# Kernel optimization log

Hardware: AMD Instinct MI355X
Metric: run time of the kernel (lower is better)

## Reference

```python
import jax, jax.numpy as jnp
import numpy as np

D = 128  # input_depth == output_depth
NUM_NODES_PATTERN = np.tile(np.array([32, 48, 64, 96], dtype=np.int64), 64)  # G=256 graphs


def _build_indices(nn_np):
    """Per pair-entry (row-major within each n_g x n_g block): global row node,
    global col node, graph id, diagonal mask; plus per-node graph id / size."""
    G = len(nn_np)
    offs = np.zeros(G, dtype=np.int64)
    offs[1:] = np.cumsum(nn_np)[:-1]
    rows_l, cols_l, g_l, diag_l = [], [], [], []
    for gi, (n, o) in enumerate(zip(nn_np, offs)):
        i = np.repeat(np.arange(n, dtype=np.int64), n)  # row index within block
        j = np.tile(np.arange(n, dtype=np.int64), n)    # col index within block
        rows_l.append(o + i)
        cols_l.append(o + j)
        g_l.append(np.full(n * n, gi, dtype=np.int64))
        diag_l.append(i == j)
    rows = np.concatenate(rows_l)
    cols = np.concatenate(cols_l)
    g_edge = np.concatenate(g_l)
    diag = np.concatenate(diag_l)
    g_node = np.repeat(np.arange(G, dtype=np.int64), nn_np)  # graph of each node
    n_node = np.repeat(nn_np, nn_np)                          # n_g of each node
    N = int(nn_np.sum())
    return rows, cols, g_edge, diag, g_node, n_node, N, G


def setup_inputs() -> dict:
    key = jax.random.key(0)
    nn_np = NUM_NODES_PATTERN
    E = int(np.sum(nn_np ** 2))  # 1,064,960 pair entries
    N = int(nn_np.sum())         # 15,360 nodes
    k1, k2, k3 = jax.random.split(key, 3)
    x = jax.random.normal(k1, (E, D), dtype=jnp.float32)
    coeffs = jax.random.normal(k2, (D, D, 5), dtype=jnp.float32) * float(np.sqrt(2.0) / (D + D))
    bias = jnp.zeros((1, D), dtype=jnp.float32)
    edges_index = jax.random.randint(k3, (2, E), 0, N, dtype=jnp.int64)  # unused by the layer
    num_nodes = jnp.asarray(nn_np)
    return {"x": x, "coeffs": coeffs, "bias": bias,
            "edges_index": edges_index, "num_nodes": num_nodes}


def reference(x, coeffs, bias, edges_index, num_nodes):
    # edges_index is unused, matching the original forward.
    nn_np = np.asarray(num_nodes)
    rows, cols, g_edge, diag, g_node, n_node, N, G = _build_indices(nn_np)
    seg = jax.ops.segment_sum
    diag_m = jnp.asarray(diag)[:, None].astype(x.dtype)  # [E,1]
    n = jnp.asarray(n_node).astype(x.dtype)[:, None]     # [N,1] block size per node

    op1 = seg(x * diag_m, jnp.asarray(rows), num_segments=N)          # diag part (unnormalized)
    op3 = seg(x, jnp.asarray(rows), num_segments=N) / n               # row sums / n
    op4 = seg(x, jnp.asarray(cols), num_segments=N) / n               # col sums / n
    diag_g = seg(x * diag_m, jnp.asarray(g_edge), num_segments=G)     # [G,d] trace per graph
    all_g = seg(x, jnp.asarray(g_edge), num_segments=G)               # [G,d] total sum per graph
    gn = jnp.asarray(g_node)
    op2 = diag_g[gn] / n                                              # trace broadcast / n
    op5 = all_g[gn] / (n * n)                                         # total broadcast / n^2

    ops = jnp.stack([op1, op2, op3, op4, op5], axis=2)                # [N, d, 5]
    out = jnp.einsum('dsb,ndb->ns', coeffs, ops) + bias               # [N, output_depth]
    return out
```

## Files before the change

### kernel.cpp

```cpp
#include <hip/hip_runtime.h>

#define D 128


__device__ __forceinline__ void f4add(float4& a, const float4& b) {
    a.x += b.x; a.y += b.y; a.z += b.z; a.w += b.w;
}

__device__ __forceinline__ void f4shflxor_add(float4& a, int mask) {
    a.x += __shfl_xor(a.x, mask);
    a.y += __shfl_xor(a.y, mask);
    a.z += __shfl_xor(a.z, mask);
    a.w += __shfl_xor(a.w, mask);
}

template<int N>
__device__ __forceinline__ void run_class(const float* __restrict__ x,
                                          long ebase, int o, int gidx, int chunk,
                                          float* __restrict__ diagG,
                                          float* __restrict__ rowG,
                                          float* __restrict__ colG,
                                          float* __restrict__ trG,
                                          float* __restrict__ totG,
                                          float4* rowpart ) {
    const int tid = threadIdx.x;
    const int L   = tid & 63;
    const int w   = tid >> 6;
    const int j0  = tid >> 3;
    const int f4  = tid & 7;
    const float invn = 1.0f / (float)N;
    constexpr bool TWO = (N > 64);
    const bool act0 = (j0 < N);
    const bool act1 = TWO && (j0 + 64 < N);

    const float4* x4 = reinterpret_cast<const float4*>(x);
    const long e0 = (ebase + j0) * 32 + chunk * 8 + f4;
    const long e1 = e0 + 64L * 32;
    const long istride = (long)N * 32;

    float4 c0 = {0,0,0,0}, c1 = {0,0,0,0};

    for (int t0 = 0; t0 < N; t0 += 16) {
#pragma unroll 8
        for (int r = 0; r < 16; ++r) {
            const int i = t0 + r;
            float4 v0 = {0,0,0,0}, v1 = {0,0,0,0};
            if (act0) v0 = x4[e0 + (long)i * istride];
            if (TWO && act1) v1 = x4[e1 + (long)i * istride];
            f4add(c0, v0);
            if (TWO) f4add(c1, v1);
            float4 s = v0;
            if (TWO) f4add(s, v1);
            f4shflxor_add(s, 8);
            f4shflxor_add(s, 16);
            f4shflxor_add(s, 32);
            if (L < 8) rowpart[(r * 8 + w) * 8 + L] = s;
        }
        __syncthreads();
        {
            const int r  = tid >> 5;
            const int dd = tid & 31;
            const float* rp = reinterpret_cast<const float*>(rowpart);
            float acc = 0.f;
#pragma unroll
            for (int w2 = 0; w2 < 8; ++w2) acc += rp[r * 256 + w2 * 32 + dd];
            rowG[(long)(o + t0 + r) * D + chunk * 32 + dd] = acc * invn;
        }
        __syncthreads();
    }

    float4 d0 = {0,0,0,0}, d1 = {0,0,0,0};
    if (act0) d0 = x4[e0 + (long)j0 * istride];
    if (TWO && act1) d1 = x4[e1 + (long)(j0 + 64) * istride];

    float4* diag4 = reinterpret_cast<float4*>(diagG);
    float4* col4  = reinterpret_cast<float4*>(colG);
    if (act0) {
        diag4[(long)(o + j0) * 32 + chunk * 8 + f4] = d0;
        col4 [(long)(o + j0) * 32 + chunk * 8 + f4] = c0;
    }
    if (TWO && act1) {
        diag4[(long)(o + j0 + 64) * 32 + chunk * 8 + f4] = d1;
        col4 [(long)(o + j0 + 64) * 32 + chunk * 8 + f4] = c1;
    }

    float4 td = d0; if (TWO) f4add(td, d1);
    float4 tc = c0; if (TWO) f4add(tc, c1);
    f4shflxor_add(td, 8);  f4shflxor_add(tc, 8);
    f4shflxor_add(td, 16); f4shflxor_add(tc, 16);
    f4shflxor_add(td, 32); f4shflxor_add(tc, 32);
    if (L < 8) {
        rowpart[w * 8 + L]      = td;
        rowpart[64 + w * 8 + L] = tc;
    }
    __syncthreads();
    float4* tr4  = reinterpret_cast<float4*>(trG);
    float4* tot4 = reinterpret_cast<float4*>(totG);
    if (tid < 8) {
        float4 a = {0,0,0,0};
#pragma unroll
        for (int w2 = 0; w2 < 8; ++w2) f4add(a, rowpart[w2 * 8 + tid]);
        tr4[gidx * 32 + chunk * 8 + tid] = a;
    } else if (tid < 16) {
        const int f = tid - 8;
        float4 a = {0,0,0,0};
#pragma unroll
        for (int w2 = 0; w2 < 8; ++w2) f4add(a, rowpart[64 + w2 * 8 + f]);
        tot4[gidx * 32 + chunk * 8 + f] = a;
    }
}

__global__ __launch_bounds__(512) void k1_reduce(const float* __restrict__ x,
                                                 float* __restrict__ diagG,
                                                 float* __restrict__ rowG,
                                                 float* __restrict__ colG,
                                                 float* __restrict__ trG,
                                                 float* __restrict__ totG) {
    __shared__ float4 rowpart[1024];

    const int b  = blockIdx.x;
    const int bb = b & 255;
    const int k  = bb >> 2;
    const int chunk = bb & 3;

    if (b < 256) {
        run_class<96>(x, 16640L * k + 7424, 240 * k + 144, 4 * k + 3, chunk, diagG, rowG, colG, trG, totG, rowpart);
    } else if (b < 512) {
        run_class<64>(x, 16640L * k + 3328, 240 * k + 80, 4 * k + 2, chunk, diagG, rowG, colG, trG, totG, rowpart);
    } else if (b < 768) {
        run_class<48>(x, 16640L * k + 1024, 240 * k + 32, 4 * k + 1, chunk, diagG, rowG, colG, trG, totG, rowpart);
    } else {
        run_class<32>(x, 16640L * k, 240 * k, 4 * k, chunk, diagG, rowG, colG, trG, totG, rowpart);
    }
}

__global__ void k0_transpose(const float* __restrict__ coeffs, float* __restrict__ Wt) {
    int d = blockIdx.x;
    int s = threadIdx.x;
    const float* cp = coeffs + ((long)d * D + s) * 5;
#pragma unroll
    for (int b = 0; b < 5; ++b) Wt[b * (D * D) + d * D + s] = cp[b];
}

__global__ __launch_bounds__(128) void k2_pg(const float* __restrict__ trG,
                                             const float* __restrict__ totG,
                                             const float* __restrict__ Wt,
                                             const float* __restrict__ bias,
                                             float* __restrict__ pg) {
    __shared__ float tr[D], tt[D];
    const int ns_[4] = {32, 48, 64, 96};
    int g = blockIdx.x;
    int c = g & 3;
    float invn = 1.0f / (float)ns_[c];

    int s = threadIdx.x;
    tr[s] = trG[g * D + s] * invn;
    tt[s] = totG[g * D + s] * invn * invn;
    __syncthreads();

    const float* W1 = Wt + 1 * D * D;
    const float* W4 = Wt + 4 * D * D;
    float acc = 0.f;
#pragma unroll 4
    for (int dd = 0; dd < D; ++dd)
        acc += W1[dd * D + s] * tr[dd] + W4[dd * D + s] * tt[dd];
    pg[g * D + s] = bias[s] + acc;
}

__global__ __launch_bounds__(512) void k3_gemm(const float* __restrict__ diagG,
                                               const float* __restrict__ rowG,
                                               const float* __restrict__ colG,
                                               const float* __restrict__ Wt,
                                               const float* __restrict__ pg,
                                               float* __restrict__ out) {
    __shared__ float ash[3][64][D];
    __shared__ int gish[64];
    const int nd0 = blockIdx.x * 64;
    const int tid = threadIdx.x;

    for (int idx = tid; idx < 64 * D; idx += 512) {
        int nn = idx >> 7;
        int d  = idx & 127;
        int nd = nd0 + nn;
        int p  = nd / 240;
        int r  = nd - p * 240;
        int c, n;
        if (r < 32)       { c = 0; n = 32; }
        else if (r < 80)  { c = 1; n = 48; }
        else if (r < 144) { c = 2; n = 64; }
        else              { c = 3; n = 96; }
        float invn = 1.0f / (float)n;
        ash[0][nn][d] = diagG[(long)nd * D + d];
        ash[1][nn][d] = rowG[(long)nd * D + d];
        ash[2][nn][d] = colG[(long)nd * D + d] * invn;
        if (d == 0) gish[nn] = 4 * p + c;
    }
    __syncthreads();

    const int s0 = tid & 31;
    const int nq = tid >> 5;
    const float* W0 = Wt;
    const float* W2 = Wt + 2 * D * D;
    const float* W3 = Wt + 3 * D * D;

    float acc[4][4];
#pragma unroll
    for (int a = 0; a < 4; ++a)
#pragma unroll
        for (int ss = 0; ss < 4; ++ss) acc[a][ss] = 0.f;

    for (int d = 0; d < D; ++d) {
        float w0[4], w2[4], w3[4];
#pragma unroll
        for (int ss = 0; ss < 4; ++ss) {
            int s = s0 + 32 * ss;
            w0[ss] = W0[d * D + s];
            w2[ss] = W2[d * D + s];
            w3[ss] = W3[d * D + s];
        }
#pragma unroll
        for (int a = 0; a < 4; ++a) {
            int nn = nq * 4 + a;
            float a0 = ash[0][nn][d];
            float a1 = ash[1][nn][d];
            float a2 = ash[2][nn][d];
#pragma unroll
            for (int ss = 0; ss < 4; ++ss)
                acc[a][ss] += w0[ss] * a0 + w2[ss] * a1 + w3[ss] * a2;
        }
    }

#pragma unroll
    for (int a = 0; a < 4; ++a) {
        int nn = nq * 4 + a;
        int nd = nd0 + nn;
        int g  = gish[nn];
#pragma unroll
        for (int ss = 0; ss < 4; ++ss) {
            int s = s0 + 32 * ss;
            out[(long)nd * D + s] = acc[a][ss] + pg[g * D + s];
        }
    }
}

extern "C" void kernel_launch(void* const* d_in, const int* in_sizes, int n_in,
                              void* d_out, int out_size, void* d_ws, size_t ws_size,
                              hipStream_t stream) {
    const float* x      = (const float*)d_in[0];
    const float* coeffs = (const float*)d_in[1];
    const float* bias   = (const float*)d_in[2];

    float* ws    = (float*)d_ws;
    float* Wt    = ws;
    float* diagG = Wt + 81920;
    float* rowG  = diagG + 1966080;
    float* colG  = rowG + 1966080;
    float* pg    = colG + 1966080;
    float* trG   = pg + 32768;
    float* totG  = trG + 32768;
    float* out   = (float*)d_out;

    k0_transpose<<<128, 128, 0, stream>>>(coeffs, Wt);
    k1_reduce<<<1024, 512, 0, stream>>>(x, diagG, rowG, colG, trG, totG);
    k2_pg<<<256, 128, 0, stream>>>(trG, totG, Wt, bias, pg);
    k3_gemm<<<240, 512, 0, stream>>>(diagG, rowG, colG, Wt, pg, out);
}
```

Measured before the change: 227.3 us.

## Use DPP lane reductions, remap reduce lanes, and vectorize GEMM with float4

The reduction kernel now remaps lanes so the per-row partial sums are combined with DPP row operations instead of cross-lane shuffles. Inactive waves for small graphs are skipped, and the occupancy hint is raised. The small GEMM kernel switches to float4 loads and stores for staging, weights, activations and outputs. Together these aim to cut shuffle latency, wasted lanes and instruction count in both kernels, at the cost of more register pressure and a more intricate lane mapping.

After: 278.5 us. 1.23x slower.

```diff
diff --git a/kernel.cpp b/kernel.cpp
--- a/kernel.cpp
+++ b/kernel.cpp
@@ -2,16 +2,33 @@
 
 #define D 128
 
+
+template<int CTRL>
+__device__ __forceinline__ float f_dpp(float v) {
+    return __int_as_float(__builtin_amdgcn_update_dpp(
+        0, __float_as_int(v), CTRL, 0xF, 0xF, true));
+}
+
+template<int CTRL>
+__device__ __forceinline__ void f4dpp_add(float4& a) {
+    a.x += f_dpp<CTRL>(a.x);
+    a.y += f_dpp<CTRL>(a.y);
+    a.z += f_dpp<CTRL>(a.z);
+    a.w += f_dpp<CTRL>(a.w);
+}
 
 __device__ __forceinline__ void f4add(float4& a, const float4& b) {
     a.x += b.x; a.y += b.y; a.z += b.z; a.w += b.w;
 }
 
-__device__ __forceinline__ void f4shflxor_add(float4& a, int mask) {
-    a.x += __shfl_xor(a.x, mask);
-    a.y += __shfl_xor(a.y, mask);
-    a.z += __shfl_xor(a.z, mask);
-    a.w += __shfl_xor(a.w, mask);
+#define DPP_X1 0xB1
+#define DPP_X2 0x4E
+#define DPP_X8 0x128
+
+__device__ __forceinline__ void f4_jreduce(float4& a) {
+    f4dpp_add<DPP_X1>(a);
+    f4dpp_add<DPP_X2>(a);
+    f4dpp_add<DPP_X8>(a);
 }
 
 template<int N>
@@ -22,16 +39,20 @@
                                           float* __restrict__ colG,
                                           float* __restrict__ trG,
                                           float* __restrict__ totG,
-                                          float4* rowpart ) {
-    const int tid = threadIdx.x;
-    const int L   = tid & 63;
-    const int w   = tid >> 6;
-    const int j0  = tid >> 3;
-    const int f4  = tid & 7;
+                                          float4* __restrict__ rowtile ,
+                                          float4* __restrict__ red     ) {
+    constexpr int NW = (N < 64 ? N / 8 : 8);
+    const int tid  = threadIdx.x;
+    const int l    = tid & 63;
+    const int w    = tid >> 6;
+    const int jsub = (l & 3) | ((l & 8) >> 1);
+    const int f4   = ((l & 4) >> 2) | ((l & 48) >> 3);
+    const int j0   = w * 8 + jsub;
+    constexpr bool TWO = (N > 64);
+    const bool act0 = (w < NW);
+    const bool act1 = TWO && (w < 4);
     const float invn = 1.0f / (float)N;
-    constexpr bool TWO = (N > 64);
-    const bool act0 = (j0 < N);
-    const bool act1 = TWO && (j0 + 64 < N);
+    const bool store8 = (jsub == 0);
 
     const float4* x4 = reinterpret_cast<const float4*>(x);
     const long e0 = (ebase + j0) * 32 + chunk * 8 + f4;
@@ -41,30 +62,32 @@
     float4 c0 = {0,0,0,0}, c1 = {0,0,0,0};
 
     for (int t0 = 0; t0 < N; t0 += 16) {
-#pragma unroll 8
-        for (int r = 0; r < 16; ++r) {
-            const int i = t0 + r;
-            float4 v0 = {0,0,0,0}, v1 = {0,0,0,0};
-            if (act0) v0 = x4[e0 + (long)i * istride];
-            if (TWO && act1) v1 = x4[e1 + (long)i * istride];
-            f4add(c0, v0);
-            if (TWO) f4add(c1, v1);
-            float4 s = v0;
-            if (TWO) f4add(s, v1);
-            f4shflxor_add(s, 8);
-            f4shflxor_add(s, 16);
-            f4shflxor_add(s, 32);
-            if (L < 8) rowpart[(r * 8 + w) * 8 + L] = s;
+        if (act0) {
+#pragma unroll
+            for (int r = 0; r < 16; ++r) {
+                const int i = t0 + r;
+                float4 v0 = x4[e0 + (long)i * istride];
+                float4 s  = v0;
+                f4add(c0, v0);
+                if (TWO && act1) {
+                    float4 v1 = x4[e1 + (long)i * istride];
+                    f4add(c1, v1);
+                    f4add(s, v1);
+                }
+                f4_jreduce(s);
+                if (store8) rowtile[(r * 8 + w) * 8 + f4] = s;
+            }
         }
         __syncthreads();
         {
-            const int r  = tid >> 5;
+            const int rr = tid >> 5;
             const int dd = tid & 31;
-            const float* rp = reinterpret_cast<const float*>(rowpart);
+            const float* rp = reinterpret_cast<const float*>(rowtile);
             float acc = 0.f;
 #pragma unroll
-            for (int w2 = 0; w2 < 8; ++w2) acc += rp[r * 256 + w2 * 32 + dd];
-            rowG[(long)(o + t0 + r) * D + chunk * 32 + dd] = acc * invn;
+            for (int w2 = 0; w2 < NW; ++w2)
+                acc += rp[(rr * 8 + w2) * 32 + dd];
+            rowG[(long)(o + t0 + rr) * D + chunk * 32 + dd] = acc * invn;
         }
         __syncthreads();
     }
@@ -84,14 +107,15 @@
         col4 [(long)(o + j0 + 64) * 32 + chunk * 8 + f4] = c1;
     }
 
-    float4 td = d0; if (TWO) f4add(td, d1);
-    float4 tc = c0; if (TWO) f4add(tc, c1);
-    f4shflxor_add(td, 8);  f4shflxor_add(tc, 8);
-    f4shflxor_add(td, 16); f4shflxor_add(tc, 16);
-    f4shflxor_add(td, 32); f4shflxor_add(tc, 32);
-    if (L < 8) {
-        rowpart[w * 8 + L]      = td;
-        rowpart[64 + w * 8 + L] = tc;
+    if (act0) {
+        float4 td = d0; if (TWO) f4add(td, d1);
+        float4 tc = c0; if (TWO) f4add(tc, c1);
+        f4_jreduce(td);
+        f4_jreduce(tc);
+        if (store8) {
+            red[w * 8 + f4]      = td;
+            red[64 + w * 8 + f4] = tc;
+        }
     }
     __syncthreads();
     float4* tr4  = reinterpret_cast<float4*>(trG);
@@ -99,24 +123,25 @@
     if (tid < 8) {
         float4 a = {0,0,0,0};
 #pragma unroll
-        for (int w2 = 0; w2 < 8; ++w2) f4add(a, rowpart[w2 * 8 + tid]);
+        for (int w2 = 0; w2 < NW; ++w2) f4add(a, red[w2 * 8 + tid]);
         tr4[gidx * 32 + chunk * 8 + tid] = a;
     } else if (tid < 16) {
         const int f = tid - 8;
         float4 a = {0,0,0,0};
 #pragma unroll
-        for (int w2 = 0; w2 < 8; ++w2) f4add(a, rowpart[64 + w2 * 8 + f]);
+        for (int w2 = 0; w2 < NW; ++w2) f4add(a, red[64 + w2 * 8 + f]);
         tot4[gidx * 32 + chunk * 8 + f] = a;
     }
 }
 
-__global__ __launch_bounds__(512) void k1_reduce(const float* __restrict__ x,
-                                                 float* __restrict__ diagG,
-                                                 float* __restrict__ rowG,
-                                                 float* __restrict__ colG,
-                                                 float* __restrict__ trG,
-                                                 float* __restrict__ totG) {
-    __shared__ float4 rowpart[1024];
+__global__ __launch_bounds__(512, 8) void k1_reduce(const float* __restrict__ x,
+                                                    float* __restrict__ diagG,
+                                                    float* __restrict__ rowG,
+                                                    float* __restrict__ colG,
+                                                    float* __restrict__ trG,
+                                                    float* __restrict__ totG) {
+    __shared__ float4 rowtile[1024];
+    __shared__ float4 red[128];
 
     const int b  = blockIdx.x;
     const int bb = b & 255;
@@ -124,13 +149,13 @@
     const int chunk = bb & 3;
 
     if (b < 256) {
-        run_class<96>(x, 16640L * k + 7424, 240 * k + 144, 4 * k + 3, chunk, diagG, rowG, colG, trG, totG, rowpart);
+        run_class<96>(x, 16640L * k + 7424, 240 * k + 144, 4 * k + 3, chunk, diagG, rowG, colG, trG, totG, rowtile, red);
     } else if (b < 512) {
-        run_class<64>(x, 16640L * k + 3328, 240 * k + 80, 4 * k + 2, chunk, diagG, rowG, colG, trG, totG, rowpart);
+        run_class<64>(x, 16640L * k + 3328, 240 * k + 80, 4 * k + 2, chunk, diagG, rowG, colG, trG, totG, rowtile, red);
     } else if (b < 768) {
-        run_class<48>(x, 16640L * k + 1024, 240 * k + 32, 4 * k + 1, chunk, diagG, rowG, colG, trG, totG, rowpart);
+        run_class<48>(x, 16640L * k + 1024, 240 * k + 32, 4 * k + 1, chunk, diagG, rowG, colG, trG, totG, rowtile, red);
     } else {
-        run_class<32>(x, 16640L * k, 240 * k, 4 * k, chunk, diagG, rowG, colG, trG, totG, rowpart);
+        run_class<32>(x, 16640L * k, 240 * k, 4 * k, chunk, diagG, rowG, colG, trG, totG, rowtile, red);
     }
 }
 
@@ -173,14 +198,18 @@
                                                const float* __restrict__ Wt,
                                                const float* __restrict__ pg,
                                                float* __restrict__ out) {
-    __shared__ float ash[3][64][D];
+    __shared__ __align__(16) float ash[3][64][D];
     __shared__ int gish[64];
     const int nd0 = blockIdx.x * 64;
     const int tid = threadIdx.x;
 
-    for (int idx = tid; idx < 64 * D; idx += 512) {
-        int nn = idx >> 7;
-        int d  = idx & 127;
+    const float4* diag4 = reinterpret_cast<const float4*>(diagG);
+    const float4* row4  = reinterpret_cast<const float4*>(rowG);
+    const float4* col4  = reinterpret_cast<const float4*>(colG);
+
+    for (int idx = tid; idx < 64 * 32; idx += 512) {
+        int nn = idx >> 5;
+        int q  = idx & 31;
         int nd = nd0 + nn;
         int p  = nd / 240;
         int r  = nd - p * 240;
@@ -190,56 +219,67 @@
         else if (r < 144) { c = 2; n = 64; }
         else              { c = 3; n = 96; }
         float invn = 1.0f / (float)n;
-        ash[0][nn][d] = diagG[(long)nd * D + d];
-        ash[1][nn][d] = rowG[(long)nd * D + d];
-        ash[2][nn][d] = colG[(long)nd * D + d] * invn;
-        if (d == 0) gish[nn] = 4 * p + c;
+        float4 dv = diag4[(long)nd * 32 + q];
+        float4 rv = row4[(long)nd * 32 + q];
+        float4 cv = col4[(long)nd * 32 + q];
+        cv.x *= invn; cv.y *= invn; cv.z *= invn; cv.w *= invn;
+        *reinterpret_cast<float4*>(&ash[0][nn][q * 4]) = dv;
+        *reinterpret_cast<float4*>(&ash[1][nn][q * 4]) = rv;
+        *reinterpret_cast<float4*>(&ash[2][nn][q * 4]) = cv;
+        if (q == 0) gish[nn] = 4 * p + c;
     }
     __syncthreads();
 
-    const int s0 = tid & 31;
+    const int s4 = tid & 31;
     const int nq = tid >> 5;
     const float* W0 = Wt;
     const float* W2 = Wt + 2 * D * D;
     const float* W3 = Wt + 3 * D * D;
 
-    float acc[4][4];
-#pragma unroll
-    for (int a = 0; a < 4; ++a)
-#pragma unroll
-        for (int ss = 0; ss < 4; ++ss) acc[a][ss] = 0.f;
-
-    for (int d = 0; d < D; ++d) {
-        float w0[4], w2[4], w3[4];
-#pragma unroll
-        for (int ss = 0; ss < 4; ++ss) {
-            int s = s0 + 32 * ss;
-            w0[ss] = W0[d * D + s];
-            w2[ss] = W2[d * D + s];
-            w3[ss] = W3[d * D + s];
+    float4 acc[4];
+#pragma unroll
+    for (int a = 0; a < 4; ++a) acc[a] = make_float4(0.f, 0.f, 0.f, 0.f);
+
+    for (int d4 = 0; d4 < 32; ++d4) {
+        float4 w0[4], w2[4], w3[4];
+#pragma unroll
+        for (int dd = 0; dd < 4; ++dd) {
+            const int d = d4 * 4 + dd;
+            w0[dd] = *reinterpret_cast<const float4*>(&W0[d * D + s4 * 4]);
+            w2[dd] = *reinterpret_cast<const float4*>(&W2[d * D + s4 * 4]);
+            w3[dd] = *reinterpret_cast<const float4*>(&W3[d * D + s4 * 4]);
         }
 #pragma unroll
         for (int a = 0; a < 4; ++a) {
-            int nn = nq * 4 + a;
-            float a0 = ash[0][nn][d];
-            float a1 = ash[1][nn][d];
-            float a2 = ash[2][nn][d];
-#pragma unroll
-            for (int ss = 0; ss < 4; ++ss)
-                acc[a][ss] += w0[ss] * a0 + w2[ss] * a1 + w3[ss] * a2;
+            const int nn = nq * 4 + a;
+            float4 a0 = *reinterpret_cast<const float4*>(&ash[0][nn][d4 * 4]);
+            float4 a1 = *reinterpret_cast<const float4*>(&ash[1][nn][d4 * 4]);
+            float4 a2 = *reinterpret_cast<const float4*>(&ash[2][nn][d4 * 4]);
+            const float* a0f = reinterpret_cast<const float*>(&a0);
+            const float* a1f = reinterpret_cast<const float*>(&a1);
+            const float* a2f = reinterpret_cast<const float*>(&a2);
+#pragma unroll
+            for (int dd = 0; dd < 4; ++dd) {
+                acc[a].x += w0[dd].x * a0f[dd] + w2[dd].x * a1f[dd] + w3[dd].x * a2f[dd];
+                acc[a].y += w0[dd].y * a0f[dd] + w2[dd].y * a1f[dd] + w3[dd].y * a2f[dd];
+                acc[a].z += w0[dd].z * a0f[dd] + w2[dd].z * a1f[dd] + w3[dd].z * a2f[dd];
+                acc[a].w += w0[dd].w * a0f[dd] + w2[dd].w * a1f[dd] + w3[dd].w * a2f[dd];
+            }
         }
     }
 
 #pragma unroll
     for (int a = 0; a < 4; ++a) {
-        int nn = nq * 4 + a;
-        int nd = nd0 + nn;
-        int g  = gish[nn];
-#pragma unroll
-        for (int ss = 0; ss < 4; ++ss) {
-            int s = s0 + 32 * ss;
-            out[(long)nd * D + s] = acc[a][ss] + pg[g * D + s];
-        }
+        const int nn = nq * 4 + a;
+        const int nd = nd0 + nn;
+        const int g  = gish[nn];
+        float4 pgv = *reinterpret_cast<const float4*>(&pg[g * D + s4 * 4]);
+        float4 r_;
+        r_.x = acc[a].x + pgv.x;
+        r_.y = acc[a].y + pgv.y;
+        r_.z = acc[a].z + pgv.z;
+        r_.w = acc[a].w + pgv.w;
+        *reinterpret_cast<float4*>(&out[(long)nd * D + s4 * 4]) = r_;
     }
 }
 
```
